# Kernel tuning notes

Measured on AMD Instinct MI355X. Metric: run time of the kernel, lower is better.

## Reference

```python
import jax, jax.numpy as jnp
import numpy as np

DIM = 4096
N_HEADS = 32
HEAD_DIM = DIM // N_HEADS
BATCH = 2
SEQ = 1024
THETA = 10000.0
NEG_INF = -1e9


def _rope_cos_sin(seq_len, head_dim):
    # NOTE: original code constructs RotatePosEmbedding with config.dim but applies
    # it per-head; the only shape-consistent interpretation (standard Llama RoPE)
    # uses head_dim frequencies, which is what we implement.
    inv_freq = 1.0 / (THETA ** (jnp.arange(0, head_dim, 2, dtype=jnp.float32) / head_dim))
    angles = jnp.arange(seq_len, dtype=jnp.float32)[:, None] * inv_freq[None, :]  # [S, hd/2]
    return jnp.cos(angles), jnp.sin(angles)


def _apply_rope(x, cos, sin):
    # x: [B,S,H,hd]; rotate consecutive pairs (complex multiply)
    B, S, H, hd = x.shape
    xr = x.reshape(B, S, H, hd // 2, 2)
    x0, x1 = xr[..., 0], xr[..., 1]
    c = cos[None, :, None, :]
    s = sin[None, :, None, :]
    out = jnp.stack([x0 * c - x1 * s, x0 * s + x1 * c], axis=-1)
    return out.reshape(B, S, H, hd)


def setup_inputs() -> dict:
    key = jax.random.key(0)
    ks = jax.random.split(key, 9)
    x = jax.random.normal(ks[0], (BATCH, SEQ, DIM), dtype=jnp.float32)
    scale = 1.0 / np.sqrt(DIM)
    wq = jax.random.normal(ks[1], (DIM, DIM), dtype=jnp.float32) * scale
    wk = jax.random.normal(ks[2], (DIM, DIM), dtype=jnp.float32) * scale
    wv = jax.random.normal(ks[3], (DIM, DIM), dtype=jnp.float32) * scale
    wo = jax.random.normal(ks[4], (DIM, DIM), dtype=jnp.float32) * scale
    bq = jax.random.normal(ks[5], (DIM,), dtype=jnp.float32) * 0.01
    bk = jax.random.normal(ks[6], (DIM,), dtype=jnp.float32) * 0.01
    bv = jax.random.normal(ks[7], (DIM,), dtype=jnp.float32) * 0.01
    bo = jax.random.normal(ks[8], (DIM,), dtype=jnp.float32) * 0.01
    # causal additive mask [S,S]
    mask = jnp.where(jnp.tril(jnp.ones((SEQ, SEQ), dtype=bool)), 0.0, NEG_INF).astype(jnp.float32)
    return {"x": x, "wq": wq, "bq": bq, "wk": wk, "bk": bk, "wv": wv, "bv": bv,
            "wo": wo, "bo": bo, "mask": mask, "start_pos": 0}


def reference(x, wq, bq, wk, bk, wv, bv, wo, bo, mask, start_pos):
    B, S, D = x.shape
    H, hd = N_HEADS, D // N_HEADS
    q = (x @ wq.T + bq).reshape(B, S, H, hd)
    k = (x @ wk.T + bk).reshape(B, S, H, hd)
    v = (x @ wv.T + bv).reshape(B, S, H, hd)
    cos, sin = _rope_cos_sin(S, hd)
    q = _apply_rope(q, cos, sin)
    k = _apply_rope(k, cos, sin)
    # start_pos == 0 prefill: cache slice [:start_pos+S] equals current k/v
    scores = jnp.einsum('bqhd,bkhd->bhqk', q, k) / np.sqrt(hd).astype(np.float32)
    scores = scores + mask[None, None, :, :]
    attn = jax.nn.softmax(scores, axis=-1)
    out = jnp.einsum('bhqk,bkhd->bqhd', attn, v).reshape(B, S, D)
    return out @ wo.T + bo
```

## Files before the change

### kernel.cpp

```cpp
#include <hip/hip_runtime.h>
#include <hip/hip_bf16.h>

#define DIM   4096
#define NH    32
#define HD    128
#define BATCH 2
#define SEQ   1024
#define MROWS (BATCH*SEQ)
#define LDQ   12288

typedef __attribute__((ext_vector_type(8))) short bf16x8;
typedef __attribute__((ext_vector_type(4))) short s16x4;
typedef __attribute__((ext_vector_type(4))) float f32x4;

__device__ inline void gload_lds16(const void* g, void* l) {
  __builtin_amdgcn_global_load_lds(
      (const __attribute__((address_space(1))) void*)g,
      (__attribute__((address_space(3))) void*)l, 16, 0, 0);
}

__device__ inline float bf2f(short b) {
  unsigned u = ((unsigned)(unsigned short)b) << 16;
  return __uint_as_float(u);
}
__device__ inline unsigned short f2bfu(float f) {
  __hip_bfloat16 h = __float2bfloat16(f);
  return *reinterpret_cast<unsigned short*>(&h);
}

__global__ void cvt_bf16_kernel(const float* __restrict__ in,
                                unsigned short* __restrict__ out, long n4) {
  long i = blockIdx.x * (long)blockDim.x + threadIdx.x;
  long stride = (long)gridDim.x * blockDim.x;
  for (; i < n4; i += stride) {
    float4 v = ((const float4*)in)[i];
    ushort4 o;
    o.x = f2bfu(v.x); o.y = f2bfu(v.y); o.z = f2bfu(v.z); o.w = f2bfu(v.w);
    ((ushort4*)out)[i] = o;
  }
}

__global__ void concat3_kernel(const float* __restrict__ a, const float* __restrict__ b,
                               const float* __restrict__ c, float* __restrict__ o) {
  int i = blockIdx.x * blockDim.x + threadIdx.x;
  if (i < 4096) o[i] = a[i];
  else if (i < 8192) o[i] = b[i - 4096];
  else if (i < 12288) o[i] = c[i - 8192];
}

__global__ void rope_table_kernel(float* __restrict__ cosT, float* __restrict__ sinT) {
  int s = blockIdx.x;
  int p = threadIdx.x;
  float inv = powf(10000.0f, -((float)(2 * p)) / 128.0f);
  float a = (float)s * inv;
  cosT[s * 64 + p] = cosf(a);
  sinT[s * 64 + p] = sinf(a);
}

__global__ void reduce_bias_kernel(const float* __restrict__ part,
                                   const float* __restrict__ bias,
                                   float* __restrict__ out) {
  long i = blockIdx.x * (long)blockDim.x + threadIdx.x;
  if (i >= (long)MROWS * DIM / 4) return;
  float4 a = ((const float4*)part)[i];
  float4 b = ((const float4*)(part + (size_t)MROWS * DIM))[i];
  float4 bb = ((const float4*)bias)[(int)(i & (DIM / 4 - 1))];
  float4 o;
  o.x = a.x + b.x + bb.x; o.y = a.y + b.y + bb.y;
  o.z = a.z + b.z + bb.z; o.w = a.w + b.w + bb.w;
  ((float4*)out)[i] = o;
}

__device__ __forceinline__ void stage_half(
    const unsigned short* __restrict__ A, const unsigned short* __restrict__ Bw,
    unsigned short* Asl, unsigned short* Bsl,
    int m0, int n0, size_t Kstr, int kcol0, int t, int half) {
#pragma unroll
  for (int j = 0; j < 2; ++j) {
    int ci = (half * 2 + j) * 512 + t;
    int r = ci >> 3, c = ci & 7;
    gload_lds16(A + (size_t)(m0 + r) * Kstr + kcol0 + ((c ^ (r & 7)) << 3), Asl + ci * 8);
  }
#pragma unroll
  for (int j = 0; j < 2; ++j) {
    int ci = (half * 2 + j) * 512 + t;
    int r = ci >> 3, c = ci & 7;
    gload_lds16(Bw + (size_t)(n0 + r) * Kstr + kcol0 + ((c ^ (r & 7)) << 3), Bsl + ci * 8);
  }
}

template <typename OutT, bool QKV_MODE>
__global__ __launch_bounds__(512, 2) void gemm_q_kernel(
    const unsigned short* __restrict__ A, const unsigned short* __restrict__ Bw,
    const float* __restrict__ bias, OutT* __restrict__ C,
    int M, int N, int Kstr, int Klen,
    const float* __restrict__ cosT, const float* __restrict__ sinT) {
  __shared__ unsigned short As[2][256 * 64];
  __shared__ unsigned short Bs[2][128 * 64 * 2];
  const int t = threadIdx.x;
  const int lane = t & 63;
  const int w = t >> 6;
  const int wm = w >> 2, wn = w & 3;
  const int np = lane & 15, hq = lane >> 4;

  int bid = blockIdx.y * gridDim.x + blockIdx.x;
  int nwg = gridDim.x * gridDim.y;
  int sb = (bid & 7) * (nwg >> 3) + (bid >> 3);
  int bx = sb % gridDim.x, by = sb / gridDim.x;
  const int m0 = by * 256, n0 = bx * 256;
  const int kb0 = blockIdx.z * Klen;
  const int NT = Klen >> 6;
  OutT* Cz = C + (size_t)blockIdx.z * M * N;

  stage_half(A, Bw, As[0], Bs[0], m0, n0, Kstr, kb0, t, 0);
  stage_half(A, Bw, As[0], Bs[0], m0, n0, Kstr, kb0, t, 1);
  stage_half(A, Bw, As[1], Bs[1], m0, n0, Kstr, kb0 + 64, t, 0);
  stage_half(A, Bw, As[1], Bs[1], m0, n0, Kstr, kb0 + 64, t, 1);

  f32x4 acc[8][4] = {};

  asm volatile("s_waitcnt vmcnt(8)" ::: "memory");
  __builtin_amdgcn_s_barrier();

  int cur = 0;
#pragma unroll 1
  for (int kt = 0; kt < NT; ++kt) {
    const unsigned short* Asl = As[cur];
    const unsigned short* Bsl = Bs[cur];
    bf16x8 af[4][2], bf[4][2];
    const int swz = np & 7;

#pragma unroll
    for (int rb = 0; rb < 4; ++rb)
#pragma unroll
      for (int kh = 0; kh < 2; ++kh)
        af[rb][kh] = *(const bf16x8*)&Asl[(wm * 128 + rb * 16 + np) * 64 +
                                          (((kh * 4 + hq) ^ swz) << 3)];
#pragma unroll
    for (int cb = 0; cb < 2; ++cb)
#pragma unroll
      for (int kh = 0; kh < 2; ++kh)
        bf[cb][kh] = *(const bf16x8*)&Bsl[(wn * 64 + cb * 16 + np) * 64 +
                                          (((kh * 4 + hq) ^ swz) << 3)];
    __builtin_amdgcn_s_barrier();
    __builtin_amdgcn_s_setprio(1);
#pragma unroll
    for (int i = 0; i < 4; ++i)
#pragma unroll
      for (int j = 0; j < 2; ++j) {
        acc[i][j] = __builtin_amdgcn_mfma_f32_16x16x32_bf16(af[i][0], bf[j][0], acc[i][j], 0, 0, 0);
        acc[i][j] = __builtin_amdgcn_mfma_f32_16x16x32_bf16(af[i][1], bf[j][1], acc[i][j], 0, 0, 0);
      }
    __builtin_amdgcn_s_setprio(0);

#pragma unroll
    for (int cb = 2; cb < 4; ++cb)
#pragma unroll
      for (int kh = 0; kh < 2; ++kh)
        bf[cb][kh] = *(const bf16x8*)&Bsl[(wn * 64 + cb * 16 + np) * 64 +
                                          (((kh * 4 + hq) ^ swz) << 3)];
    __builtin_amdgcn_s_barrier();
    __builtin_amdgcn_s_setprio(1);
#pragma unroll
    for (int i = 0; i < 4; ++i)
#pragma unroll
      for (int j = 0; j < 2; ++j) {
        acc[i][j + 2] = __builtin_amdgcn_mfma_f32_16x16x32_bf16(af[i][0], bf[j + 2][0], acc[i][j + 2], 0, 0, 0);
        acc[i][j + 2] = __builtin_amdgcn_mfma_f32_16x16x32_bf16(af[i][1], bf[j + 2][1], acc[i][j + 2], 0, 0, 0);
      }
    __builtin_amdgcn_s_setprio(0);

#pragma unroll
    for (int rb = 0; rb < 4; ++rb)
#pragma unroll
      for (int kh = 0; kh < 2; ++kh)
        af[rb][kh] = *(const bf16x8*)&Asl[(wm * 128 + 64 + rb * 16 + np) * 64 +
                                          (((kh * 4 + hq) ^ swz) << 3)];
    asm volatile("s_waitcnt lgkmcnt(0)" ::: "memory");
    __builtin_amdgcn_sched_barrier(0);
    __builtin_amdgcn_s_barrier();
    if (kt + 2 < NT)
      stage_half(A, Bw, As[cur], Bs[cur], m0, n0, Kstr, kb0 + ((kt + 2) << 6), t, 0);
    __builtin_amdgcn_s_setprio(1);
#pragma unroll
    for (int i = 0; i < 4; ++i)
#pragma unroll
      for (int j = 0; j < 2; ++j) {
        acc[i + 4][j] = __builtin_amdgcn_mfma_f32_16x16x32_bf16(af[i][0], bf[j][0], acc[i + 4][j], 0, 0, 0);
        acc[i + 4][j] = __builtin_amdgcn_mfma_f32_16x16x32_bf16(af[i][1], bf[j][1], acc[i + 4][j], 0, 0, 0);
      }
    __builtin_amdgcn_s_setprio(0);

    if (kt + 2 < NT)
      stage_half(A, Bw, As[cur], Bs[cur], m0, n0, Kstr, kb0 + ((kt + 2) << 6), t, 1);
    __builtin_amdgcn_s_barrier();
    __builtin_amdgcn_s_setprio(1);
#pragma unroll
    for (int i = 0; i < 4; ++i)
#pragma unroll
      for (int j = 0; j < 2; ++j) {
        acc[i + 4][j + 2] = __builtin_amdgcn_mfma_f32_16x16x32_bf16(af[i][0], bf[j + 2][0], acc[i + 4][j + 2], 0, 0, 0);
        acc[i + 4][j + 2] = __builtin_amdgcn_mfma_f32_16x16x32_bf16(af[i][1], bf[j + 2][1], acc[i + 4][j + 2], 0, 0, 0);
      }
    __builtin_amdgcn_s_setprio(0);
    if (kt + 2 < NT) {
      asm volatile("s_waitcnt vmcnt(8)" ::: "memory");
    } else {
      asm volatile("s_waitcnt vmcnt(0)" ::: "memory");
    }
    __builtin_amdgcn_s_barrier();
    cur ^= 1;
  }

  const int orow0 = m0 + wm * 128;
  const int ocol0 = n0 + wn * 64 + np;
  const bool do_rope = QKV_MODE && (n0 < 8192);
#pragma unroll
  for (int j = 0; j < 4; ++j) {
    const int col = ocol0 + j * 16;
    float bj = QKV_MODE ? bias[col] : 0.0f;
    const int p0 = (col & 127) >> 1;
    const bool even = (lane & 1) == 0;
#pragma unroll
    for (int i = 0; i < 8; ++i) {
#pragma unroll
      for (int r = 0; r < 4; ++r) {
        int orow = orow0 + i * 16 + hq * 4 + r;
        float v = acc[i][j][r] + bj;
        if (do_rope) {
          int srow = orow & (SEQ - 1);
          float c = cosT[srow * 64 + p0];
          float s = sinT[srow * 64 + p0];
          float pv = __shfl_xor(v, 1);
          v = even ? (v * c - pv * s) : (pv * s + v * c);
        }
        size_t off = (size_t)orow * N + col;
        if constexpr (sizeof(OutT) == 2)
          ((unsigned short*)Cz)[off] = f2bfu(v);
        else
          ((float*)Cz)[off] = v;
      }
    }
  }
}

__global__ __launch_bounds__(256, 1) void flash_attn_kernel(
    const unsigned short* __restrict__ QKV, unsigned short* __restrict__ O) {
  __shared__ unsigned short Ks[64 * 128];
  __shared__ unsigned short Vt[128 * 64];
  __shared__ unsigned short Ps[4][32 * 64];

  const int p  = blockIdx.x;
  const int bh = blockIdx.y;
  const int b  = bh >> 5;
  const int hh = bh & 31;
  const int t    = threadIdx.x;
  const int lane = t & 63;
  const int w    = t >> 6;
  const int np   = lane & 15;
  const int hq   = lane >> 4;

  const size_t rowbase = (size_t)b * SEQ * LDQ;
  const unsigned short* Qg = QKV + rowbase + (size_t)hh * HD;
  const unsigned short* Kg = QKV + rowbase + 4096 + (size_t)hh * HD;
  const unsigned short* Vg = QKV + rowbase + 8192 + (size_t)hh * HD;
  unsigned short* Og = O + (size_t)b * SEQ * DIM + (size_t)hh * HD;

  const int krow = t >> 2;
  const int kc0  = (t & 3) * 32;
  const int vr0  = (t & 15) * 4;
  const int vc0  = (t >> 4) * 8;

  unsigned short* Pw = &Ps[w][0];
  const float SCALE = 0.08838834764831843f;

  bf16x8 vk[4], vv[4];

#pragma unroll 1
  for (int pass = 0; pass < 2; ++pass) {
    const int qt    = pass ? (7 - p) : p;
    const int nt    = 2 * qt + 2;
    const int qbase = qt * 128 + w * 32;

    bf16x8 qf[2][4];
#pragma unroll
    for (int rb = 0; rb < 2; ++rb)
#pragma unroll
      for (int kb = 0; kb < 4; ++kb)
        qf[rb][kb] = *(const bf16x8*)&Qg[(size_t)(qbase + rb * 16 + np) * LDQ + kb * 32 + hq * 8];

    f32x4 acc[2][8] = {};
    float m_run[2][4], l_run[2][4];
#pragma unroll
    for (int rb = 0; rb < 2; ++rb)
#pragma unroll
      for (int r = 0; r < 4; ++r) { m_run[rb][r] = -3.0e38f; l_run[rb][r] = 0.0f; }

    {
      const unsigned short* kp = Kg + (size_t)krow * LDQ + kc0;
      const unsigned short* vp = Vg + (size_t)vr0 * LDQ + vc0;
#pragma unroll
      for (int jj = 0; jj < 4; ++jj) vk[jj] = *(const bf16x8*)(kp + jj * 8);
#pragma unroll
      for (int jj = 0; jj < 4; ++jj) vv[jj] = *(const bf16x8*)(vp + (size_t)jj * LDQ);
    }

#pragma unroll 1
    for (int kt = 0; kt < nt; ++kt) {
      __syncthreads();

#pragma unroll
      for (int jj = 0; jj < 4; ++jj) {
        int c = (t & 3) * 4 + jj;
        *(bf16x8*)((char*)Ks + krow * 256 + ((c ^ (krow & 7)) << 4)) = vk[jj];
      }
#pragma unroll
      for (int i = 0; i < 8; ++i) {
        int col = vc0 + i;
        s16x4 sv;
        sv[0] = vv[0][i]; sv[1] = vv[1][i]; sv[2] = vv[2][i]; sv[3] = vv[3][i];
        *(s16x4*)((char*)Vt + ((col * 128 + vr0 * 2) ^ ((col & 7) << 4))) = sv;
      }
      __syncthreads();

      if (kt + 1 < nt) {
        const unsigned short* kp = Kg + (size_t)((kt + 1) * 64 + krow) * LDQ + kc0;
        const unsigned short* vp = Vg + (size_t)((kt + 1) * 64 + vr0) * LDQ + vc0;
#pragma unroll
        for (int jj = 0; jj < 4; ++jj) vk[jj] = *(const bf16x8*)(kp + jj * 8);
#pragma unroll
        for (int jj = 0; jj < 4; ++jj) vv[jj] = *(const bf16x8*)(vp + (size_t)jj * LDQ);
      }

      f32x4 sc[4][2] = {};
#pragma unroll
      for (int ct = 0; ct < 4; ++ct) {
#pragma unroll
        for (int kb = 0; kb < 4; ++kb) {
          bf16x8 kf = *(const bf16x8*)((char*)Ks + (ct * 16 + np) * 256 +
                                       (((kb * 4 + hq) ^ (np & 7)) << 4));
          sc[ct][0] = __builtin_amdgcn_mfma_f32_16x16x32_bf16(qf[0][kb], kf, sc[ct][0], 0, 0, 0);
          sc[ct][1] = __builtin_amdgcn_mfma_f32_16x16x32_bf16(qf[1][kb], kf, sc[ct][1], 0, 0, 0);
        }
      }

      const bool maskt = (kt >= 2 * qt);
#pragma unroll
      for (int ct = 0; ct < 4; ++ct) {
        int kvc = kt * 64 + ct * 16 + np;
#pragma unroll
        for (int rb = 0; rb < 2; ++rb)
#pragma unroll
          for (int r = 0; r < 4; ++r) {
            float v = sc[ct][rb][r] * SCALE;
            if (maskt && kvc > qbase + rb * 16 + hq * 4 + r) v = -1.0e9f;
            sc[ct][rb][r] = v;
          }
      }

      float sf[2][4];
#pragma unroll
      for (int rb = 0; rb < 2; ++rb)
#pragma unroll
        for (int r = 0; r < 4; ++r) {
          float tmax = fmaxf(fmaxf(sc[0][rb][r], sc[1][rb][r]),
                             fmaxf(sc[2][rb][r], sc[3][rb][r]));
          tmax = fmaxf(tmax, __shfl_xor(tmax, 1));
          tmax = fmaxf(tmax, __shfl_xor(tmax, 2));
          tmax = fmaxf(tmax, __shfl_xor(tmax, 4));
          tmax = fmaxf(tmax, __shfl_xor(tmax, 8));
          float mn = fmaxf(m_run[rb][r], tmax);
          sf[rb][r] = __expf(m_run[rb][r] - mn);
          m_run[rb][r] = mn;
        }

#pragma unroll
      for (int rb = 0; rb < 2; ++rb)
#pragma unroll
        for (int r = 0; r < 4; ++r) {
          int prow = rb * 16 + hq * 4 + r;
          int swz = (prow & 7) << 4;
          float rsum = 0.f;
#pragma unroll
          for (int ct = 0; ct < 4; ++ct) {
            float pv = __expf(sc[ct][rb][r] - m_run[rb][r]);
            rsum += pv;
            *(unsigned short*)((char*)Pw + ((prow * 128 + (ct * 16 + np) * 2) ^ swz)) = f2bfu(pv);
          }
          rsum += __shfl_xor(rsum, 1);
          rsum += __shfl_xor(rsum, 2);
          rsum += __shfl_xor(rsum, 4);
          rsum += __shfl_xor(rsum, 8);
          l_run[rb][r] = l_run[rb][r] * sf[rb][r] + rsum;
        }

#pragma unroll
      for (int rb = 0; rb < 2; ++rb)
#pragma unroll
        for (int nt2 = 0; nt2 < 8; ++nt2)
#pragma unroll
          for (int r = 0; r < 4; ++r)
            acc[rb][nt2][r] *= sf[rb][r];

#pragma unroll
      for (int kb2 = 0; kb2 < 2; ++kb2) {
        bf16x8 pa0 = *(const bf16x8*)((char*)Pw +
            (((0 * 16 + np) * 128 + kb2 * 64 + hq * 16) ^ ((np & 7) << 4)));
        bf16x8 pa1 = *(const bf16x8*)((char*)Pw +
            (((1 * 16 + np) * 128 + kb2 * 64 + hq * 16) ^ ((np & 7) << 4)));
#pragma unroll
        for (int nt2 = 0; nt2 < 8; ++nt2) {
          int col = nt2 * 16 + np;
          bf16x8 vf = *(const bf16x8*)((char*)Vt +
              ((col * 128 + kb2 * 64 + hq * 16) ^ ((col & 7) << 4)));
          acc[0][nt2] = __builtin_amdgcn_mfma_f32_16x16x32_bf16(pa0, vf, acc[0][nt2], 0, 0, 0);
          acc[1][nt2] = __builtin_amdgcn_mfma_f32_16x16x32_bf16(pa1, vf, acc[1][nt2], 0, 0, 0);
        }
      }
    }

#pragma unroll
    for (int rb = 0; rb < 2; ++rb)
#pragma unroll
      for (int r = 0; r < 4; ++r) {
        float rl = 1.0f / l_run[rb][r];
        int orow = qbase + rb * 16 + hq * 4 + r;
#pragma unroll
        for (int nt2 = 0; nt2 < 8; ++nt2)
          Og[(size_t)orow * DIM + nt2 * 16 + np] = f2bfu(acc[rb][nt2][r] * rl);
      }
  }
}

extern "C" void kernel_launch(void* const* d_in, const int* in_sizes, int n_in,
                              void* d_out, int out_size, void* d_ws, size_t ws_size,
                              hipStream_t stream) {
  const float* x  = (const float*)d_in[0];
  const float* wq = (const float*)d_in[1];
  const float* bq = (const float*)d_in[2];
  const float* wk = (const float*)d_in[3];
  const float* bk = (const float*)d_in[4];
  const float* wv = (const float*)d_in[5];
  const float* bv = (const float*)d_in[6];
  const float* wo = (const float*)d_in[7];
  const float* bo = (const float*)d_in[8];
  float* out = (float*)d_out;

  char* ws = (char*)d_ws;
  unsigned short* wqkvb = (unsigned short*)(ws);
  float* part           = (float*)(ws);
  unsigned short* wob   = (unsigned short*)(ws + (96ll  << 20));
  unsigned short* xb    = (unsigned short*)(ws + (128ll << 20));
  unsigned short* qkv   = (unsigned short*)(ws + (144ll << 20));
  unsigned short* ab    = (unsigned short*)(ws + (192ll << 20));
  float* biasqkv = (float*)(ws + (208ll << 20));
  float* cosT    = (float*)(ws + (208ll << 20) + (64  << 10));
  float* sinT    = (float*)(ws + (208ll << 20) + (320 << 10));

  cvt_bf16_kernel<<<2048, 256, 0, stream>>>(x,  xb, (long)MROWS * DIM / 4);
  cvt_bf16_kernel<<<2048, 256, 0, stream>>>(wq, wqkvb,                        (long)DIM * DIM / 4);
  cvt_bf16_kernel<<<2048, 256, 0, stream>>>(wk, wqkvb + (size_t)DIM * DIM,    (long)DIM * DIM / 4);
  cvt_bf16_kernel<<<2048, 256, 0, stream>>>(wv, wqkvb + 2 * (size_t)DIM * DIM,(long)DIM * DIM / 4);
  cvt_bf16_kernel<<<2048, 256, 0, stream>>>(wo, wob, (long)DIM * DIM / 4);

  concat3_kernel<<<48, 256, 0, stream>>>(bq, bk, bv, biasqkv);
  rope_table_kernel<<<SEQ, 64, 0, stream>>>(cosT, sinT);

  dim3 gq(LDQ / 256, MROWS / 256, 1);
  gemm_q_kernel<unsigned short, true><<<gq, 512, 0, stream>>>(
      xb, wqkvb, biasqkv, qkv, MROWS, LDQ, DIM, DIM, cosT, sinT);

  dim3 ga(4, BATCH * NH);
  flash_attn_kernel<<<ga, 256, 0, stream>>>(qkv, ab);

  dim3 go(DIM / 256, MROWS / 256, 2);
  gemm_q_kernel<float, false><<<go, 512, 0, stream>>>(
      ab, wob, nullptr, part, MROWS, DIM, DIM, DIM / 2, nullptr, nullptr);

  reduce_bias_kernel<<<(MROWS * DIM / 4 + 255) / 256, 256, 0, stream>>>(part, bo, out);
}
```

Baseline: 567.2 us.

## Template GEMM N-tile and use 192-wide tiles for QKV projection

Parameterizes the bf16 GEMM's N tile width and restructures its staging into separate A/B loads interleaved with MFMA phases, with wait counts derived from the tile size. The QKV projection now uses 192-column tiles, giving 512 workgroups instead of 384 to fill the GPU's two-blocks-per-CU slots evenly. It moves the RoPE shuffle outside the branch and decides RoPE per column, since tiles no longer align to the Q/K/V boundaries. Narrower tiles reduce per-block reuse of A.

```diff
diff --git a/kernel.cpp b/kernel.cpp
--- a/kernel.cpp
+++ b/kernel.cpp
@@ -26,6 +26,12 @@
 __device__ inline unsigned short f2bfu(float f) {
   __hip_bfloat16 h = __float2bfloat16(f);
   return *reinterpret_cast<unsigned short*>(&h);
+}
+
+template <int N> __device__ __forceinline__ void wait_vm() {
+  if constexpr (N == 0)      asm volatile("s_waitcnt vmcnt(0)" ::: "memory");
+  else if constexpr (N == 7) asm volatile("s_waitcnt vmcnt(7)" ::: "memory");
+  else                       asm volatile("s_waitcnt vmcnt(8)" ::: "memory");
 }
 
 __global__ void cvt_bf16_kernel(const float* __restrict__ in,
@@ -71,32 +77,18 @@
   ((float4*)out)[i] = o;
 }
 
-__device__ __forceinline__ void stage_half(
-    const unsigned short* __restrict__ A, const unsigned short* __restrict__ Bw,
-    unsigned short* Asl, unsigned short* Bsl,
-    int m0, int n0, size_t Kstr, int kcol0, int t, int half) {
-#pragma unroll
-  for (int j = 0; j < 2; ++j) {
-    int ci = (half * 2 + j) * 512 + t;
-    int r = ci >> 3, c = ci & 7;
-    gload_lds16(A + (size_t)(m0 + r) * Kstr + kcol0 + ((c ^ (r & 7)) << 3), Asl + ci * 8);
-  }
-#pragma unroll
-  for (int j = 0; j < 2; ++j) {
-    int ci = (half * 2 + j) * 512 + t;
-    int r = ci >> 3, c = ci & 7;
-    gload_lds16(Bw + (size_t)(n0 + r) * Kstr + kcol0 + ((c ^ (r & 7)) << 3), Bsl + ci * 8);
-  }
-}
-
-template <typename OutT, bool QKV_MODE>
+template <typename OutT, bool QKV_MODE, int NB>
 __global__ __launch_bounds__(512, 2) void gemm_q_kernel(
     const unsigned short* __restrict__ A, const unsigned short* __restrict__ Bw,
     const float* __restrict__ bias, OutT* __restrict__ C,
     int M, int N, int Kstr, int Klen,
     const float* __restrict__ cosT, const float* __restrict__ sinT) {
+  constexpr int CBF = NB / 64;
+  constexpr int BL  = NB / 64;
+  constexpr int VM  = 4 + BL;
+  constexpr int WNC = NB / 4;
   __shared__ unsigned short As[2][256 * 64];
-  __shared__ unsigned short Bs[2][128 * 64 * 2];
+  __shared__ unsigned short Bs[2][NB * 64];
   const int t = threadIdx.x;
   const int lane = t & 63;
   const int w = t >> 6;
@@ -107,19 +99,34 @@
   int nwg = gridDim.x * gridDim.y;
   int sb = (bid & 7) * (nwg >> 3) + (bid >> 3);
   int bx = sb % gridDim.x, by = sb / gridDim.x;
-  const int m0 = by * 256, n0 = bx * 256;
+  const int m0 = by * 256, n0 = bx * NB;
   const int kb0 = blockIdx.z * Klen;
   const int NT = Klen >> 6;
   OutT* Cz = C + (size_t)blockIdx.z * M * N;
 
-  stage_half(A, Bw, As[0], Bs[0], m0, n0, Kstr, kb0, t, 0);
-  stage_half(A, Bw, As[0], Bs[0], m0, n0, Kstr, kb0, t, 1);
-  stage_half(A, Bw, As[1], Bs[1], m0, n0, Kstr, kb0 + 64, t, 0);
-  stage_half(A, Bw, As[1], Bs[1], m0, n0, Kstr, kb0 + 64, t, 1);
-
-  f32x4 acc[8][4] = {};
-
-  asm volatile("s_waitcnt vmcnt(8)" ::: "memory");
+  auto stageA2 = [&](unsigned short* Asl, int kcol0, int j0) {
+#pragma unroll
+    for (int j = j0; j < j0 + 2; ++j) {
+      int ci = j * 512 + t;
+      int r = ci >> 3, c = ci & 7;
+      gload_lds16(A + (size_t)(m0 + r) * Kstr + kcol0 + ((c ^ (r & 7)) << 3), Asl + ci * 8);
+    }
+  };
+  auto stageB = [&](unsigned short* Bsl, int kcol0) {
+#pragma unroll
+    for (int j = 0; j < BL; ++j) {
+      int ci = j * 512 + t;
+      int r = ci >> 3, c = ci & 7;
+      gload_lds16(Bw + (size_t)(n0 + r) * Kstr + kcol0 + ((c ^ (r & 7)) << 3), Bsl + ci * 8);
+    }
+  };
+
+  stageA2(As[0], kb0, 0); stageA2(As[0], kb0, 2); stageB(Bs[0], kb0);
+  stageA2(As[1], kb0 + 64, 0); stageA2(As[1], kb0 + 64, 2); stageB(Bs[1], kb0 + 64);
+
+  f32x4 acc[8][CBF] = {};
+
+  wait_vm<VM>();
   __builtin_amdgcn_s_barrier();
 
   int cur = 0;
@@ -127,20 +134,22 @@
   for (int kt = 0; kt < NT; ++kt) {
     const unsigned short* Asl = As[cur];
     const unsigned short* Bsl = Bs[cur];
-    bf16x8 af[4][2], bf[4][2];
     const int swz = np & 7;
+    const int kn = kb0 + ((kt + 2) << 6);
+    const bool more = (kt + 2 < NT);
+    bf16x8 al[4][2], ah[4][2], bf[CBF][2];
 
 #pragma unroll
     for (int rb = 0; rb < 4; ++rb)
 #pragma unroll
       for (int kh = 0; kh < 2; ++kh)
-        af[rb][kh] = *(const bf16x8*)&Asl[(wm * 128 + rb * 16 + np) * 64 +
+        al[rb][kh] = *(const bf16x8*)&Asl[(wm * 128 + rb * 16 + np) * 64 +
                                           (((kh * 4 + hq) ^ swz) << 3)];
 #pragma unroll
-    for (int cb = 0; cb < 2; ++cb)
+    for (int cb = 0; cb < CBF; ++cb)
 #pragma unroll
       for (int kh = 0; kh < 2; ++kh)
-        bf[cb][kh] = *(const bf16x8*)&Bsl[(wn * 64 + cb * 16 + np) * 64 +
+        bf[cb][kh] = *(const bf16x8*)&Bsl[(wn * WNC + cb * 16 + np) * 64 +
                                           (((kh * 4 + hq) ^ swz) << 3)];
     __builtin_amdgcn_s_barrier();
     __builtin_amdgcn_s_setprio(1);
@@ -148,90 +157,80 @@
     for (int i = 0; i < 4; ++i)
 #pragma unroll
       for (int j = 0; j < 2; ++j) {
-        acc[i][j] = __builtin_amdgcn_mfma_f32_16x16x32_bf16(af[i][0], bf[j][0], acc[i][j], 0, 0, 0);
-        acc[i][j] = __builtin_amdgcn_mfma_f32_16x16x32_bf16(af[i][1], bf[j][1], acc[i][j], 0, 0, 0);
+        acc[i][j] = __builtin_amdgcn_mfma_f32_16x16x32_bf16(al[i][0], bf[j][0], acc[i][j], 0, 0, 0);
+        acc[i][j] = __builtin_amdgcn_mfma_f32_16x16x32_bf16(al[i][1], bf[j][1], acc[i][j], 0, 0, 0);
       }
     __builtin_amdgcn_s_setprio(0);
 
 #pragma unroll
-    for (int cb = 2; cb < 4; ++cb)
+    for (int rb = 0; rb < 4; ++rb)
 #pragma unroll
       for (int kh = 0; kh < 2; ++kh)
-        bf[cb][kh] = *(const bf16x8*)&Bsl[(wn * 64 + cb * 16 + np) * 64 +
-                                          (((kh * 4 + hq) ^ swz) << 3)];
-    __builtin_amdgcn_s_barrier();
-    __builtin_amdgcn_s_setprio(1);
-#pragma unroll
-    for (int i = 0; i < 4; ++i)
-#pragma unroll
-      for (int j = 0; j < 2; ++j) {
-        acc[i][j + 2] = __builtin_amdgcn_mfma_f32_16x16x32_bf16(af[i][0], bf[j + 2][0], acc[i][j + 2], 0, 0, 0);
-        acc[i][j + 2] = __builtin_amdgcn_mfma_f32_16x16x32_bf16(af[i][1], bf[j + 2][1], acc[i][j + 2], 0, 0, 0);
-      }
-    __builtin_amdgcn_s_setprio(0);
-
-#pragma unroll
-    for (int rb = 0; rb < 4; ++rb)
-#pragma unroll
-      for (int kh = 0; kh < 2; ++kh)
-        af[rb][kh] = *(const bf16x8*)&Asl[(wm * 128 + 64 + rb * 16 + np) * 64 +
+        ah[rb][kh] = *(const bf16x8*)&Asl[(wm * 128 + 64 + rb * 16 + np) * 64 +
                                           (((kh * 4 + hq) ^ swz) << 3)];
     asm volatile("s_waitcnt lgkmcnt(0)" ::: "memory");
     __builtin_amdgcn_sched_barrier(0);
     __builtin_amdgcn_s_barrier();
-    if (kt + 2 < NT)
-      stage_half(A, Bw, As[cur], Bs[cur], m0, n0, Kstr, kb0 + ((kt + 2) << 6), t, 0);
+    if (more) stageA2(As[cur], kn, 0);
     __builtin_amdgcn_s_setprio(1);
 #pragma unroll
     for (int i = 0; i < 4; ++i)
 #pragma unroll
+      for (int j = 2; j < CBF; ++j) {
+        acc[i][j] = __builtin_amdgcn_mfma_f32_16x16x32_bf16(al[i][0], bf[j][0], acc[i][j], 0, 0, 0);
+        acc[i][j] = __builtin_amdgcn_mfma_f32_16x16x32_bf16(al[i][1], bf[j][1], acc[i][j], 0, 0, 0);
+      }
+    __builtin_amdgcn_s_setprio(0);
+    __builtin_amdgcn_s_barrier();
+
+    if (more) stageA2(As[cur], kn, 2);
+    __builtin_amdgcn_s_setprio(1);
+#pragma unroll
+    for (int i = 0; i < 4; ++i)
+#pragma unroll
       for (int j = 0; j < 2; ++j) {
-        acc[i + 4][j] = __builtin_amdgcn_mfma_f32_16x16x32_bf16(af[i][0], bf[j][0], acc[i + 4][j], 0, 0, 0);
-        acc[i + 4][j] = __builtin_amdgcn_mfma_f32_16x16x32_bf16(af[i][1], bf[j][1], acc[i + 4][j], 0, 0, 0);
+        acc[i + 4][j] = __builtin_amdgcn_mfma_f32_16x16x32_bf16(ah[i][0], bf[j][0], acc[i + 4][j], 0, 0, 0);
+        acc[i + 4][j] = __builtin_amdgcn_mfma_f32_16x16x32_bf16(ah[i][1], bf[j][1], acc[i + 4][j], 0, 0, 0);
       }
     __builtin_amdgcn_s_setprio(0);
-
-    if (kt + 2 < NT)
-      stage_half(A, Bw, As[cur], Bs[cur], m0, n0, Kstr, kb0 + ((kt + 2) << 6), t, 1);
     __builtin_amdgcn_s_barrier();
+
+    if (more) stageB(Bs[cur], kn);
     __builtin_amdgcn_s_setprio(1);
 #pragma unroll
     for (int i = 0; i < 4; ++i)
 #pragma unroll
-      for (int j = 0; j < 2; ++j) {
-        acc[i + 4][j + 2] = __builtin_amdgcn_mfma_f32_16x16x32_bf16(af[i][0], bf[j + 2][0], acc[i + 4][j + 2], 0, 0, 0);
-        acc[i + 4][j + 2] = __builtin_amdgcn_mfma_f32_16x16x32_bf16(af[i][1], bf[j + 2][1], acc[i + 4][j + 2], 0, 0, 0);
+      for (int j = 2; j < CBF; ++j) {
+        acc[i + 4][j] = __builtin_amdgcn_mfma_f32_16x16x32_bf16(ah[i][0], bf[j][0], acc[i + 4][j], 0, 0, 0);
+        acc[i + 4][j] = __builtin_amdgcn_mfma_f32_16x16x32_bf16(ah[i][1], bf[j][1], acc[i + 4][j], 0, 0, 0);
       }
     __builtin_amdgcn_s_setprio(0);
-    if (kt + 2 < NT) {
-      asm volatile("s_waitcnt vmcnt(8)" ::: "memory");
-    } else {
-      asm volatile("s_waitcnt vmcnt(0)" ::: "memory");
-    }
+    if (more) wait_vm<VM>();
+    else      wait_vm<0>();
     __builtin_amdgcn_s_barrier();
     cur ^= 1;
   }
 
   const int orow0 = m0 + wm * 128;
-  const int ocol0 = n0 + wn * 64 + np;
-  const bool do_rope = QKV_MODE && (n0 < 8192);
-#pragma unroll
-  for (int j = 0; j < 4; ++j) {
+  const int ocol0 = n0 + wn * WNC + np;
+#pragma unroll
+  for (int j = 0; j < CBF; ++j) {
     const int col = ocol0 + j * 16;
     float bj = QKV_MODE ? bias[col] : 0.0f;
     const int p0 = (col & 127) >> 1;
     const bool even = (lane & 1) == 0;
+    const bool do_rope = QKV_MODE && (col < 8192);
 #pragma unroll
     for (int i = 0; i < 8; ++i) {
 #pragma unroll
       for (int r = 0; r < 4; ++r) {
         int orow = orow0 + i * 16 + hq * 4 + r;
         float v = acc[i][j][r] + bj;
+        float pv = __shfl_xor(v, 1);
         if (do_rope) {
           int srow = orow & (SEQ - 1);
           float c = cosT[srow * 64 + p0];
           float s = sinT[srow * 64 + p0];
-          float pv = __shfl_xor(v, 1);
           v = even ? (v * c - pv * s) : (pv * s + v * c);
         }
         size_t off = (size_t)orow * N + col;
@@ -466,15 +465,15 @@
   concat3_kernel<<<48, 256, 0, stream>>>(bq, bk, bv, biasqkv);
   rope_table_kernel<<<SEQ, 64, 0, stream>>>(cosT, sinT);
 
-  dim3 gq(LDQ / 256, MROWS / 256, 1);
-  gemm_q_kernel<unsigned short, true><<<gq, 512, 0, stream>>>(
+  dim3 gq(LDQ / 192, MROWS / 256, 1);
+  gemm_q_kernel<unsigned short, true, 192><<<gq, 512, 0, stream>>>(
       xb, wqkvb, biasqkv, qkv, MROWS, LDQ, DIM, DIM, cosT, sinT);
 
   dim3 ga(4, BATCH * NH);
   flash_attn_kernel<<<ga, 256, 0, stream>>>(qkv, ab);
 
   dim3 go(DIM / 256, MROWS / 256, 2);
-  gemm_q_kernel<float, false><<<go, 512, 0, stream>>>(
+  gemm_q_kernel<float, false, 256><<<go, 512, 0, stream>>>(
       ab, wob, nullptr, part, MROWS, DIM, DIM, DIM / 2, nullptr, nullptr);
 
   reduce_bias_kernel<<<(MROWS * DIM / 4 + 255) / 256, 256, 0, stream>>>(part, bo, out);
```

Result: faster. 529.2 us (-6.7%).
